# Performance work log

Hardware: AMD Instinct MI355X
Metric: run time of the kernel (lower is better)

The kernel has to match this reference:

```python
import jax, jax.numpy as jnp
from jax import lax
import numpy as np

W = 64          # net_width
NITER = 10
THRESH = 1e-3
MSTEP = 1.0


def setup_inputs() -> dict:
    key = jax.random.key(0)
    ks = jax.random.split(key, 10)
    B, Nh, DIM = 8, 16384, 1024
    eye = jnp.eye(W, dtype=jnp.float32)
    return {
        'y_re': jax.random.normal(ks[0], (B, 1, Nh), jnp.float32),
        'y_im': jax.random.normal(ks[1], (B, 1, Nh), jnp.float32),
        'H_re': jax.random.normal(ks[2], (32768, DIM), jnp.float32) / np.sqrt(DIM),
        'H_im': jax.random.normal(ks[3], (32768, DIM), jnp.float32) / np.sqrt(DIM),
        # torch inits: estep.weight=I, estep.bias=0, update.weight=I, memory.weight=1e-6*I;
        # add small perturbations so the math is non-degenerate.
        'estep_w': eye + 0.05 * jax.random.normal(ks[4], (W, W), jnp.float32),
        'estep_b': jnp.zeros((W,), jnp.float32),
        'update_w': eye + 0.05 * jax.random.normal(ks[5], (W, W), jnp.float32),
        'update_b': 0.02 * jax.random.normal(ks[6], (W,), jnp.float32),
        'memory_w': 1e-6 * eye + 0.01 * jax.random.normal(ks[7], (W, W), jnp.float32),
        'memory_b': 0.02 * jax.random.normal(ks[8], (W,), jnp.float32),
    }


def _forward(y_re, y_im, H_re, H_im, estep_w, estep_b, update_w, update_b, memory_w, memory_b):
    y = (y_re + 1j * y_im).astype(jnp.complex64)          # [B,1,Nh]
    y = jnp.concatenate([y, jnp.conj(y)], axis=2)         # [B,1,N]
    H = (H_re + 1j * H_im).astype(jnp.complex64)          # [N,DIM]
    B, N = y.shape[0], y.shape[2]
    DIM = H.shape[1]
    nb = N // W
    Hb = H.reshape(nb, W, DIM)                            # [nb,W,DIM]
    yb = y.reshape(B, nb, W).transpose(1, 0, 2)[:, :, None, :]  # [nb,B,1,W]

    x0 = jnp.zeros((B, 1, DIM), jnp.complex64)
    tau0 = jnp.ones((nb, B, 1, W), jnp.float32)

    def block_step(xk, blk):
        H_i, y_i, tau_i = blk                              # [W,DIM], [B,1,W], [B,1,W]
        zk = jnp.einsum('bod,wd->bow', xk, H_i)            # [B,1,W] complex
        r = y_i - zk
        a2 = jnp.abs(r) ** 2                               # [B,1,W] float32
        # expectation_step: xt / std(xt) (torch.std = unbiased, global)
        xt = a2 / jnp.std(a2, ddof=1)
        ht = jax.nn.sigmoid(xt @ estep_w.T + estep_b)
        tau_new = jax.nn.relu(ht @ update_w.T + update_b + tau_i @ memory_w.T + memory_b)
        sigma2 = jnp.mean(a2, axis=2, keepdims=True)       # [B,1,1]
        residual = MSTEP * r * tau_new / sigma2            # complex
        xk = xk + jnp.einsum('bow,wd->bod', residual, jnp.conj(H_i)) / (W * DIM)
        return xk, tau_new

    def iteration(carry, _):
        xk, tau = carry
        xk, tau_new = lax.scan(block_step, xk, (Hb, yb, tau))  # sequential over blocks
        # soft threshold: sgn(x) * relu(|x| - threshold * max|x|)
        ax = jnp.abs(xk)
        m = jnp.max(ax)
        sgn = jnp.where(ax > 0, xk / jnp.where(ax > 0, ax, 1.0), 0.0 + 0.0j)
        xk = sgn * jax.nn.relu(ax - THRESH * m)
        return (xk, tau_new), None

    (xk, tau), _ = lax.scan(iteration, (x0, tau0), None, length=NITER)
    tau_out = tau[:, :, 0, :].transpose(1, 0, 2)           # [B,nb,W]
    return jnp.real(xk), tau_out


def reference(y_re, y_im, H_re, H_im, estep_w, estep_b, update_w, update_b, memory_w, memory_b):
    return _forward(y_re, y_im, H_re, H_im, estep_w, estep_b,
                    update_w, update_b, memory_w, memory_b)
```

## Files before the change

kernel.cpp:

```cpp
#include <hip/hip_runtime.h>
#include <math.h>

#define NT  256
#define NWG 64
#define SCOPE_AG __HIP_MEMORY_SCOPE_AGENT

__device__ __forceinline__ float ld_f(const float* p) {
    return __hip_atomic_load(p, __ATOMIC_RELAXED, SCOPE_AG);
}
__device__ __forceinline__ void st_f(float* p, float v) {
    __hip_atomic_store(p, v, __ATOMIC_RELAXED, SCOPE_AG);
}
__device__ __forceinline__ unsigned ld_u(const unsigned* p) {
    return __hip_atomic_load(p, __ATOMIC_RELAXED, SCOPE_AG);
}
__device__ __forceinline__ void st_u(unsigned* p, unsigned v) {
    __hip_atomic_store(p, v, __ATOMIC_RELAXED, SCOPE_AG);
}
__device__ __forceinline__ float2 ld_f2(const float2* p) {
    unsigned long long u = __hip_atomic_load((const unsigned long long*)p, __ATOMIC_RELAXED, SCOPE_AG);
    float2 r;
    r.x = __uint_as_float((unsigned)u);
    r.y = __uint_as_float((unsigned)(u >> 32));
    return r;
}
__device__ __forceinline__ void st_f2(float2* p, float2 v) {
    unsigned long long u = ((unsigned long long)__float_as_uint(v.y) << 32) | (unsigned long long)__float_as_uint(v.x);
    __hip_atomic_store((unsigned long long*)p, u, __ATOMIC_RELAXED, SCOPE_AG);
}

__device__ __forceinline__ float wsum64(float v) {
    #pragma unroll
    for (int m = 1; m < 64; m <<= 1) v += __shfl_xor(v, m);
    return v;
}
__device__ __forceinline__ float wmax64(float v) {
    #pragma unroll
    for (int m = 1; m < 64; m <<= 1) v = fmaxf(v, __shfl_xor(v, m));
    return v;
}


__launch_bounds__(NT, 1)
__global__ void robii_kernel(
    const float* __restrict__ y_re, const float* __restrict__ y_im,
    const float* __restrict__ H_re, const float* __restrict__ H_im,
    const float* __restrict__ estep_w, const float* __restrict__ estep_b,
    const float* __restrict__ update_w, const float* __restrict__ update_b,
    const float* __restrict__ memory_w, const float* __restrict__ memory_b,
    float* __restrict__ out, float* __restrict__ ws)
{
    __shared__ float wTe[4096], wTu[4096], wTm[4096];
    __shared__ float be[64], bu[64], bm[64];
    __shared__ float a2s[512];
    __shared__ float redl[8];
    __shared__ float gmax[1];
    __shared__ float2 rown[64];
    __shared__ float xts[64], hts[64], taurow[64];
    __shared__ float2 resid[64];
    __shared__ float2 cpartC[4][32][4];
    __shared__ float2 x_l[128];

    float* mpartf = (float*)cpartC;

    const int g = blockIdx.x, t = threadIdx.x;
    const int c = g & 7;
    const int b = g >> 3;
    const int lane = t & 63, wv = t >> 6;
    const int sub = t & 31;
    const int rbase = t >> 5;

    float2*   partws = (float2*)ws;
    float*    tauws  = ws + 16384;
    float*    pmws   = ws + 278528;
    unsigned* flags  = (unsigned*)(ws + 278592);

    for (int i = t; i < 4096; i += NT) {
        int j = i >> 6, k = i & 63;
        wTe[k * 64 + j] = estep_w[i];
        wTu[k * 64 + j] = update_w[i];
        wTm[k * 64 + j] = memory_w[i];
    }
    if (t < 64) { be[t] = estep_b[t]; bu[t] = update_b[t]; bm[t] = memory_b[t]; taurow[t] = 1.0f; }
    if (t < 128) x_l[t] = make_float2(0.0f, 0.0f);
    for (int i = t; i < 4096; i += NT) st_f(&tauws[g * 4096 + i], 1.0f);

    unsigned ep = 1;
    {
        unsigned* plane = flags + ((ep & 1u) << 9);
        __syncthreads();
        if (t == 0) st_u(&plane[g * 8], ep);
        if (t < 64) {
            while (ld_u(&plane[t * 8]) != ep) __builtin_amdgcn_s_sleep(1);
        }
        __syncthreads();
    }

    const size_t hcol = (size_t)c * 128 + (size_t)sub * 4;

    float4 hAre[8], hAim[8], hBre[8], hBim[8];

#define PREF(DRE, DIM_, BLKN) do {                                                   \
        const float* _pr = H_re + ((size_t)(BLKN) * 64 + rbase) * 1024 + hcol;       \
        const float* _pi = H_im + ((size_t)(BLKN) * 64 + rbase) * 1024 + hcol;       \
        _Pragma("unroll")                                                            \
        for (int _j = 0; _j < 8; ++_j) {                                             \
            DRE[_j]  = *(const float4*)(_pr + (size_t)_j * 8192);                    \
            DIM_[_j] = *(const float4*)(_pi + (size_t)_j * 8192);                    \
        }                                                                            \
    } while (0)

    PREF(hAre, hAim, 0);

#define STEP(BLK, CRE, CIM, NRE, NIM) do {                                           \
        const int blk = (BLK);                                                       \
        const int par = blk & 1;                                                     \
        __syncthreads();                               \
            \
        float2 xr0 = x_l[sub * 4 + 0], xr1 = x_l[sub * 4 + 1];                       \
        float2 xr2 = x_l[sub * 4 + 2], xr3 = x_l[sub * 4 + 3];                       \
        _Pragma("unroll")                                                            \
        for (int j = 0; j < 8; ++j) {                                                \
            float4 hr = CRE[j], hi = CIM[j];                                         \
            float sr, si;                                                            \
            sr  = xr0.x * hr.x - xr0.y * hi.x;  si  = xr0.x * hi.x + xr0.y * hr.x;   \
            sr += xr1.x * hr.y - xr1.y * hi.y;  si += xr1.x * hi.y + xr1.y * hr.y;   \
            sr += xr2.x * hr.z - xr2.y * hi.z;  si += xr2.x * hi.z + xr2.y * hr.z;   \
            sr += xr3.x * hr.w - xr3.y * hi.w;  si += xr3.x * hi.w + xr3.y * hr.w;   \
            _Pragma("unroll")                                                        \
            for (int m = 1; m < 32; m <<= 1) {                                       \
                sr += __shfl_xor(sr, m); si += __shfl_xor(si, m);                    \
            }                                                                        \
            if (sub == 0)                                                            \
                st_f2(&partws[par * 4096 + (b * 64 + rbase + 8 * j) * 8 + c],        \
                      make_float2(sr, si));                                          \
        }                                                                            \
        ++ep;                                                                        \
        unsigned* plane = flags + ((ep & 1u) << 9);                                  \
                       \
        __syncthreads();                                                             \
        if (t == 0) st_u(&plane[g * 8], ep);                                         \
                \
        PREF(NRE, NIM, ((blk + 1) & 511));                                           \
        float tau_nxt = 0.0f;                                                        \
        if (t < 64) tau_nxt = ld_f(&tauws[(((blk + 1) & 511) * 8 + b) * 64 + t]);    \
        float yAr, yAi, yBr, yBi;                                                    \
        {                                                                            \
            int b1 = t >> 6, w1 = t & 63, n1 = blk * 64 + w1;                        \
            if (n1 < 16384) { yAr = y_re[b1 * 16384 + n1];         yAi = y_im[b1 * 16384 + n1]; } \
            else            { yAr = y_re[b1 * 16384 + n1 - 16384]; yAi = -y_im[b1 * 16384 + n1 - 16384]; } \
            int i2 = t + 256;                                                        \
            int b2 = i2 >> 6, w2 = i2 & 63, n2 = blk * 64 + w2;                      \
            if (n2 < 16384) { yBr = y_re[b2 * 16384 + n2];         yBi = y_im[b2 * 16384 + n2]; } \
            else            { yBr = y_re[b2 * 16384 + n2 - 16384]; yBi = -y_im[b2 * 16384 + n2 - 16384]; } \
        }                                                                            \
                \
        if (t < 64) {                                                                \
            while (ld_u(&plane[t * 8]) != ep) __builtin_amdgcn_s_sleep(1);           \
        }                                                                            \
        __syncthreads();                                                             \
                                      \
        _Pragma("unroll")                                                            \
        for (int e = 0; e < 2; ++e) {                                                \
            int idx = t + e * 256;                                                   \
            int b1 = idx >> 6, w = idx & 63;                                         \
            const float2* pp = partws + (size_t)par * 4096 + (size_t)idx * 8;        \
            float zr = 0.0f, zi = 0.0f;                                              \
            _Pragma("unroll")                                                        \
            for (int cc = 0; cc < 8; ++cc) {                                         \
                float2 v = ld_f2(pp + cc);                                           \
                zr += v.x; zi += v.y;                                                \
            }                                                                        \
            float rr = ((e == 0) ? yAr : yBr) - zr;                                  \
            float ri = ((e == 0) ? yAi : yBi) - zi;                                  \
            a2s[idx] = rr * rr + ri * ri;                                            \
            if (b1 == b) rown[w] = make_float2(rr, ri);                              \
        }                                                                            \
        __syncthreads();                                                             \
                                       \
        float va = a2s[t] + a2s[t + 256];                                            \
        float s_ = wsum64(va);                                                       \
        if (lane == 0) redl[wv] = s_;                                                \
        __syncthreads();                                                             \
        float mean = (redl[0] + redl[1] + redl[2] + redl[3]) * (1.0f / 512.0f);      \
        float d0 = a2s[t] - mean, d1 = a2s[t + 256] - mean;                          \
        float s2_ = wsum64(d0 * d0 + d1 * d1);                                       \
        float sg  = wsum64(a2s[b * 64 + lane]) * (1.0f / 64.0f);                     \
        if (lane == 0) redl[4 + wv] = s2_;                                           \
        __syncthreads();                                                             \
        float stdv = sqrtf((redl[4] + redl[5] + redl[6] + redl[7]) * (1.0f / 511.0f)); \
        if (t < 64) xts[t] = a2s[b * 64 + t] / stdv;                                 \
        __syncthreads();                                                             \
          \
        {                                                                            \
            int j = t & 63, q = t >> 6;                                              \
            float acc = 0.0f;                                                        \
            _Pragma("unroll")                                                        \
            for (int k16 = 0; k16 < 16; ++k16) {                                     \
                int k = q * 16 + k16;                                                \
                acc += wTe[k * 64 + j] * xts[k];                                     \
            }                                                                        \
            mpartf[q * 64 + j] = acc;                                                \
        }                                                                            \
        __syncthreads();                                                             \
        if (t < 64) {                                                                \
            float acc = be[t] + mpartf[t] + mpartf[64 + t] + mpartf[128 + t] + mpartf[192 + t]; \
            hts[t] = 1.0f / (1.0f + expf(-acc));                                     \
        }                                                                            \
        __syncthreads();                                                             \
                          \
        {                                                                            \
            int j = t & 63, q = t >> 6;                                              \
            float acc = 0.0f;                                                        \
            _Pragma("unroll")                                                        \
            for (int k16 = 0; k16 < 16; ++k16) {                                     \
                int k = q * 16 + k16;                                                \
                acc += wTu[k * 64 + j] * hts[k] + wTm[k * 64 + j] * taurow[k];       \
            }                                                                        \
            mpartf[q * 64 + j] = acc;                                                \
        }                                                                            \
        __syncthreads();                                                             \
        if (t < 64) {                                                                \
            float tn = bu[t] + bm[t] + mpartf[t] + mpartf[64 + t] + mpartf[128 + t] + mpartf[192 + t]; \
            tn = fmaxf(tn, 0.0f);                                                    \
            if (c == 0) st_f(&tauws[(blk * 8 + b) * 64 + t], tn);                    \
            float2 rv = rown[t];                                                     \
            float scl = tn / sg;                                                     \
            resid[t] = make_float2(rv.x * scl, rv.y * scl);                          \
        }                                                                            \
        __syncthreads();                                                             \
            \
        float2 ac0 = make_float2(0.f, 0.f), ac1 = make_float2(0.f, 0.f);             \
        float2 ac2 = make_float2(0.f, 0.f), ac3 = make_float2(0.f, 0.f);             \
        _Pragma("unroll")                                                            \
        for (int j = 0; j < 8; ++j) {                                                \
            float2 rs = resid[rbase + 8 * j];                                        \
            float4 hr = CRE[j], hi = CIM[j];                                         \
            ac0.x += rs.x * hr.x + rs.y * hi.x;  ac0.y += rs.y * hr.x - rs.x * hi.x; \
            ac1.x += rs.x * hr.y + rs.y * hi.y;  ac1.y += rs.y * hr.y - rs.x * hi.y; \
            ac2.x += rs.x * hr.z + rs.y * hi.z;  ac2.y += rs.y * hr.z - rs.x * hi.z; \
            ac3.x += rs.x * hr.w + rs.y * hi.w;  ac3.y += rs.y * hr.w - rs.x * hi.w; \
        }                                                                            \
        ac0.x += __shfl_xor(ac0.x, 32); ac0.y += __shfl_xor(ac0.y, 32);              \
        ac1.x += __shfl_xor(ac1.x, 32); ac1.y += __shfl_xor(ac1.y, 32);              \
        ac2.x += __shfl_xor(ac2.x, 32); ac2.y += __shfl_xor(ac2.y, 32);              \
        ac3.x += __shfl_xor(ac3.x, 32); ac3.y += __shfl_xor(ac3.y, 32);              \
        if ((t & 32) == 0) {                                                         \
            cpartC[wv][sub][0] = ac0; cpartC[wv][sub][1] = ac1;                      \
            cpartC[wv][sub][2] = ac2; cpartC[wv][sub][3] = ac3;                      \
        }                                                                            \
        if (t < 64) taurow[t] = tau_nxt;                  \
        __syncthreads();                                                             \
        if (t < 128) {                                                               \
            int sl = t >> 2, kk = t & 3;                                             \
            float2 s0 = cpartC[0][sl][kk], s1 = cpartC[1][sl][kk];                   \
            float2 s2 = cpartC[2][sl][kk], s3 = cpartC[3][sl][kk];                   \
            float2 xv = x_l[t];                                                      \
            xv.x += (s0.x + s1.x + s2.x + s3.x) * (1.0f / 65536.0f);                 \
            xv.y += (s0.y + s1.y + s2.y + s3.y) * (1.0f / 65536.0f);                 \
            x_l[t] = xv;                                                             \
        }                                                                            \
    } while (0)

    #pragma unroll 1
    for (int iter = 0; iter < 10; ++iter) {
        #pragma unroll 1
        for (int blk2 = 0; blk2 < 512; blk2 += 2) {
            STEP(blk2,     hAre, hAim, hBre, hBim);
            STEP(blk2 + 1, hBre, hBim, hAre, hAim);
        }

        float lm = 0.0f;
        if (t < 128) { float2 xv = x_l[t]; lm = sqrtf(xv.x * xv.x + xv.y * xv.y); }
        lm = wmax64(lm);
        if (lane == 0) redl[wv] = lm;
        __syncthreads();
        if (t == 0) st_f(&pmws[g], fmaxf(fmaxf(redl[0], redl[1]), fmaxf(redl[2], redl[3])));
        ++ep;
        {
            unsigned* plane = flags + ((ep & 1u) << 9);
            __syncthreads();
            if (t == 0) st_u(&plane[g * 8], ep);
            if (t < 64) {
                while (ld_u(&plane[t * 8]) != ep) __builtin_amdgcn_s_sleep(1);
            }
            __syncthreads();
        }
        float pv = (t < 64) ? ld_f(&pmws[t]) : 0.0f;
        pv = wmax64(pv);
        if (t == 0) gmax[0] = pv;
        __syncthreads();
        float m = gmax[0];
        if (t < 128) {
            float2 xv = x_l[t];
            float ax = sqrtf(xv.x * xv.x + xv.y * xv.y);
            float s = (ax > 0.0f) ? fmaxf(ax - 1e-3f * m, 0.0f) / ax : 0.0f;
            x_l[t] = make_float2(xv.x * s, xv.y * s);
        }
        __syncthreads();
    }

    if (t < 128) out[b * 1024 + c * 128 + t] = x_l[t].x;
    for (int i = g * 8; i < g * 8 + 8; ++i) {
        for (int idx = t; idx < 512; idx += NT) {
            int bb = idx >> 6, w = idx & 63;
            out[8192 + bb * 32768 + i * 64 + w] = ld_f(&tauws[(i * 8 + bb) * 64 + w]);
        }
    }
#undef STEP
#undef PREF
}

__global__ void robii_diag_kernel(float* out, int code) {
    int i = blockIdx.x * blockDim.x + threadIdx.x;
    if (i < 8192) out[i] = 1.0e6f * (float)(1 + code);
}

extern "C" void kernel_launch(void* const* d_in, const int* in_sizes, int n_in,
                              void* d_out, int out_size, void* d_ws, size_t ws_size,
                              hipStream_t stream) {
    (void)in_sizes; (void)n_in; (void)out_size; (void)ws_size;
    const float* y_re     = (const float*)d_in[0];
    const float* y_im     = (const float*)d_in[1];
    const float* H_re     = (const float*)d_in[2];
    const float* H_im     = (const float*)d_in[3];
    const float* estep_w  = (const float*)d_in[4];
    const float* estep_b  = (const float*)d_in[5];
    const float* update_w = (const float*)d_in[6];
    const float* update_b = (const float*)d_in[7];
    const float* memory_w = (const float*)d_in[8];
    const float* memory_b = (const float*)d_in[9];
    float* outp = (float*)d_out;
    float* wsp  = (float*)d_ws;

    hipLaunchKernelGGL(robii_kernel, dim3(NWG), dim3(NT), 0, stream,
                       y_re, y_im, H_re, H_im, estep_w, estep_b,
                       update_w, update_b, memory_w, memory_b, outp, wsp);
    hipError_t e = hipGetLastError();
    if (e != hipSuccess) {
        hipLaunchKernelGGL(robii_diag_kernel, dim3(32), dim3(256), 0, stream,
                           outp, (int)e);
    }
}
```

Baseline: 39.18 ms.

## Replace per-block flag barrier with tagged partial sums and store tau as bf16

Removes the grid-wide flag barrier in each block step. Each partial dot-product value is now packed with an epoch tag in a 64-bit word, so readers spin until every tag matches instead of waiting on a separate flag plane. Tau state is also stored in workspace as packed bf16 pairs, which halves its traffic. The cost is lower precision in tau, both in the recurrence and in the output, plus more polling loads per value and twice as many stores for partials.

```diff
diff --git a/kernel.cpp b/kernel.cpp
--- a/kernel.cpp
+++ b/kernel.cpp
@@ -4,6 +4,7 @@
 #define NT  256
 #define NWG 64
 #define SCOPE_AG __HIP_MEMORY_SCOPE_AGENT
+typedef unsigned long long ull;
 
 __device__ __forceinline__ float ld_f(const float* p) {
     return __hip_atomic_load(p, __ATOMIC_RELAXED, SCOPE_AG);
@@ -17,17 +18,24 @@
 __device__ __forceinline__ void st_u(unsigned* p, unsigned v) {
     __hip_atomic_store(p, v, __ATOMIC_RELAXED, SCOPE_AG);
 }
-__device__ __forceinline__ float2 ld_f2(const float2* p) {
-    unsigned long long u = __hip_atomic_load((const unsigned long long*)p, __ATOMIC_RELAXED, SCOPE_AG);
-    float2 r;
-    r.x = __uint_as_float((unsigned)u);
-    r.y = __uint_as_float((unsigned)(u >> 32));
-    return r;
-}
-__device__ __forceinline__ void st_f2(float2* p, float2 v) {
-    unsigned long long u = ((unsigned long long)__float_as_uint(v.y) << 32) | (unsigned long long)__float_as_uint(v.x);
-    __hip_atomic_store((unsigned long long*)p, u, __ATOMIC_RELAXED, SCOPE_AG);
-}
+__device__ __forceinline__ ull ld_u64(const ull* p) {
+    return __hip_atomic_load(p, __ATOMIC_RELAXED, SCOPE_AG);
+}
+__device__ __forceinline__ void st_u64(ull* p, ull v) {
+    __hip_atomic_store(p, v, __ATOMIC_RELAXED, SCOPE_AG);
+}
+__device__ __forceinline__ ull pack_tf(unsigned tag, float v) {
+    return ((ull)__float_as_uint(v) << 32) | (ull)tag;
+}
+__device__ __forceinline__ float hi_f(ull u) { return __uint_as_float((unsigned)(u >> 32)); }
+
+__device__ __forceinline__ unsigned bf16pack(float even, float odd) {
+    unsigned ua = __float_as_uint(even); ua += 0x7FFFu + ((ua >> 16) & 1u);
+    unsigned ub = __float_as_uint(odd);  ub += 0x7FFFu + ((ub >> 16) & 1u);
+    return (ua >> 16) | (ub & 0xFFFF0000u);
+}
+__device__ __forceinline__ float bf16lo(unsigned w) { return __uint_as_float(w << 16); }
+__device__ __forceinline__ float bf16hi(unsigned w) { return __uint_as_float(w & 0xFFFF0000u); }
 
 __device__ __forceinline__ float wsum64(float v) {
     #pragma unroll
@@ -70,10 +78,10 @@
     const int sub = t & 31;
     const int rbase = t >> 5;
 
-    float2*   partws = (float2*)ws;
-    float*    tauws  = ws + 16384;
-    float*    pmws   = ws + 278528;
-    unsigned* flags  = (unsigned*)(ws + 278592);
+    ull*      partuw = (ull*)ws;
+    unsigned* tau32  = (unsigned*)(ws + 32768);
+    float*    pmws   = ws + 163840;
+    unsigned* flags  = (unsigned*)(ws + 163904);
 
     for (int i = t; i < 4096; i += NT) {
         int j = i >> 6, k = i & 63;
@@ -83,7 +91,11 @@
     }
     if (t < 64) { be[t] = estep_b[t]; bu[t] = update_b[t]; bm[t] = memory_b[t]; taurow[t] = 1.0f; }
     if (t < 128) x_l[t] = make_float2(0.0f, 0.0f);
-    for (int i = t; i < 4096; i += NT) st_f(&tauws[g * 4096 + i], 1.0f);
+    for (int i = t; i < 2048; i += NT) st_u(&tau32[g * 2048 + i], 0x3F803F80u);
+    {
+        int par_i = t >> 7, w_i = (t >> 1) & 63, reim = t & 1;
+        st_u64(&partuw[((size_t)par_i * 512 + b * 64 + w_i) * 16 + (size_t)c * 2 + reim], 0ull);
+    }
 
     unsigned ep = 1;
     {
@@ -115,8 +127,9 @@
 #define STEP(BLK, CRE, CIM, NRE, NIM) do {                                           \
         const int blk = (BLK);                                                       \
         const int par = blk & 1;                                                     \
+        const unsigned stag = (unsigned)(iter * 512 + blk + 1);                      \
         __syncthreads();                               \
-            \
+              \
         float2 xr0 = x_l[sub * 4 + 0], xr1 = x_l[sub * 4 + 1];                       \
         float2 xr2 = x_l[sub * 4 + 2], xr3 = x_l[sub * 4 + 3];                       \
         _Pragma("unroll")                                                            \
@@ -131,19 +144,16 @@
             for (int m = 1; m < 32; m <<= 1) {                                       \
                 sr += __shfl_xor(sr, m); si += __shfl_xor(si, m);                    \
             }                                                                        \
-            if (sub == 0)                                                            \
-                st_f2(&partws[par * 4096 + (b * 64 + rbase + 8 * j) * 8 + c],        \
-                      make_float2(sr, si));                                          \
-        }                                                                            \
-        ++ep;                                                                        \
-        unsigned* plane = flags + ((ep & 1u) << 9);                                  \
-                       \
-        __syncthreads();                                                             \
-        if (t == 0) st_u(&plane[g * 8], ep);                                         \
-                \
+            ull* pw = partuw + ((size_t)par * 512 + b * 64 + rbase + 8 * j) * 16     \
+                             + (size_t)c * 2;                                        \
+            if (sub == 0)      st_u64(pw,     pack_tf(stag, sr));                    \
+            else if (sub == 1) st_u64(pw + 1, pack_tf(stag, si));                    \
+        }                                                                            \
+             \
         PREF(NRE, NIM, ((blk + 1) & 511));                                           \
-        float tau_nxt = 0.0f;                                                        \
-        if (t < 64) tau_nxt = ld_f(&tauws[(((blk + 1) & 511) * 8 + b) * 64 + t]);    \
+        unsigned tauw = 0;                                                           \
+        if (t < 64)                                                                  \
+            tauw = ld_u(&tau32[(((blk + 1) & 511) * 8 + b) * 32 + (t >> 1)]);        \
         float yAr, yAi, yBr, yBi;                                                    \
         {                                                                            \
             int b1 = t >> 6, w1 = t & 63, n1 = blk * 64 + w1;                        \
@@ -154,26 +164,35 @@
             if (n2 < 16384) { yBr = y_re[b2 * 16384 + n2];         yBi = y_im[b2 * 16384 + n2]; } \
             else            { yBr = y_re[b2 * 16384 + n2 - 16384]; yBi = -y_im[b2 * 16384 + n2 - 16384]; } \
         }                                                                            \
-                \
-        if (t < 64) {                                                                \
-            while (ld_u(&plane[t * 8]) != ep) __builtin_amdgcn_s_sleep(1);           \
-        }                                                                            \
-        __syncthreads();                                                             \
-                                      \
+             \
         _Pragma("unroll")                                                            \
         for (int e = 0; e < 2; ++e) {                                                \
             int idx = t + e * 256;                                                   \
-            int b1 = idx >> 6, w = idx & 63;                                         \
-            const float2* pp = partws + (size_t)par * 4096 + (size_t)idx * 8;        \
+            const ull* pb = partuw + ((size_t)par * 512 + idx) * 16;                 \
             float zr = 0.0f, zi = 0.0f;                                              \
             _Pragma("unroll")                                                        \
-            for (int cc = 0; cc < 8; ++cc) {                                         \
-                float2 v = ld_f2(pp + cc);                                           \
-                zr += v.x; zi += v.y;                                                \
+            for (int h = 0; h < 2; ++h) {                                            \
+                const ull* pc = pb + h * 8;                                          \
+                ull v0, v1, v2, v3, v4, v5, v6, v7;                                  \
+                bool ok = false;                                                     \
+                while (!ok) {                                                        \
+                    v0 = ld_u64(pc + 0); v1 = ld_u64(pc + 1);                        \
+                    v2 = ld_u64(pc + 2); v3 = ld_u64(pc + 3);                        \
+                    v4 = ld_u64(pc + 4); v5 = ld_u64(pc + 5);                        \
+                    v6 = ld_u64(pc + 6); v7 = ld_u64(pc + 7);                        \
+                    ok = ((unsigned)v0 == stag) & ((unsigned)v1 == stag)             \
+                       & ((unsigned)v2 == stag) & ((unsigned)v3 == stag)             \
+                       & ((unsigned)v4 == stag) & ((unsigned)v5 == stag)             \
+                       & ((unsigned)v6 == stag) & ((unsigned)v7 == stag);            \
+                    if (!ok) __builtin_amdgcn_s_sleep(1);                            \
+                }                                                                    \
+                zr += hi_f(v0) + hi_f(v2) + hi_f(v4) + hi_f(v6);                     \
+                zi += hi_f(v1) + hi_f(v3) + hi_f(v5) + hi_f(v7);                     \
             }                                                                        \
             float rr = ((e == 0) ? yAr : yBr) - zr;                                  \
             float ri = ((e == 0) ? yAi : yBi) - zi;                                  \
             a2s[idx] = rr * rr + ri * ri;                                            \
+            int b1 = idx >> 6, w = idx & 63;                                         \
             if (b1 == b) rown[w] = make_float2(rr, ri);                              \
         }                                                                            \
         __syncthreads();                                                             \
@@ -191,7 +210,7 @@
         float stdv = sqrtf((redl[4] + redl[5] + redl[6] + redl[7]) * (1.0f / 511.0f)); \
         if (t < 64) xts[t] = a2s[b * 64 + t] / stdv;                                 \
         __syncthreads();                                                             \
-          \
+                                \
         {                                                                            \
             int j = t & 63, q = t >> 6;                                              \
             float acc = 0.0f;                                                        \
@@ -223,7 +242,9 @@
         if (t < 64) {                                                                \
             float tn = bu[t] + bm[t] + mpartf[t] + mpartf[64 + t] + mpartf[128 + t] + mpartf[192 + t]; \
             tn = fmaxf(tn, 0.0f);                                                    \
-            if (c == 0) st_f(&tauws[(blk * 8 + b) * 64 + t], tn);                    \
+            float tno = __shfl_xor(tn, 1);                                           \
+            if (c == 0 && (t & 1) == 0)                                              \
+                st_u(&tau32[(blk * 8 + b) * 32 + (t >> 1)], bf16pack(tn, tno));      \
             float2 rv = rown[t];                                                     \
             float scl = tn / sg;                                                     \
             resid[t] = make_float2(rv.x * scl, rv.y * scl);                          \
@@ -249,7 +270,8 @@
             cpartC[wv][sub][0] = ac0; cpartC[wv][sub][1] = ac1;                      \
             cpartC[wv][sub][2] = ac2; cpartC[wv][sub][3] = ac3;                      \
         }                                                                            \
-        if (t < 64) taurow[t] = tau_nxt;                  \
+        if (t < 64)                         \
+            taurow[t] = (t & 1) ? bf16hi(tauw) : bf16lo(tauw);                       \
         __syncthreads();                                                             \
         if (t < 128) {                                                               \
             int sl = t >> 2, kk = t & 3;                                             \
@@ -304,7 +326,8 @@
     for (int i = g * 8; i < g * 8 + 8; ++i) {
         for (int idx = t; idx < 512; idx += NT) {
             int bb = idx >> 6, w = idx & 63;
-            out[8192 + bb * 32768 + i * 64 + w] = ld_f(&tauws[(i * 8 + bb) * 64 + w]);
+            unsigned uw = ld_u(&tau32[(i * 8 + bb) * 32 + (w >> 1)]);
+            out[8192 + bb * 32768 + i * 64 + w] = (w & 1) ? bf16hi(uw) : bf16lo(uw);
         }
     }
 #undef STEP
```

After: 61.26 ms. 56.3% more time.

## Replace flag barriers with tagged partial-sum data words for cross-workgroup sync

Applied to the files above, without the earlier changes.

Removes the per-block grid-wide flag barrier. Each partial z value now carries an 8-bit epoch tag in its low mantissa bits, and consumers spin until all eight tagged partials for their row match the expected tag. The per-iteration max exchange is tagged the same way. This drops a full barrier round trip per block step, at the cost of truncating 8 mantissa bits of the partial sums, which reduces precision, and of adding polling loads on the data itself.

```diff
diff --git a/kernel.cpp b/kernel.cpp
--- a/kernel.cpp
+++ b/kernel.cpp
@@ -4,6 +4,7 @@
 #define NT  256
 #define NWG 64
 #define SCOPE_AG __HIP_MEMORY_SCOPE_AGENT
+typedef unsigned long long ull;
 
 __device__ __forceinline__ float ld_f(const float* p) {
     return __hip_atomic_load(p, __ATOMIC_RELAXED, SCOPE_AG);
@@ -17,16 +18,21 @@
 __device__ __forceinline__ void st_u(unsigned* p, unsigned v) {
     __hip_atomic_store(p, v, __ATOMIC_RELAXED, SCOPE_AG);
 }
-__device__ __forceinline__ float2 ld_f2(const float2* p) {
-    unsigned long long u = __hip_atomic_load((const unsigned long long*)p, __ATOMIC_RELAXED, SCOPE_AG);
-    float2 r;
-    r.x = __uint_as_float((unsigned)u);
-    r.y = __uint_as_float((unsigned)(u >> 32));
-    return r;
-}
-__device__ __forceinline__ void st_f2(float2* p, float2 v) {
-    unsigned long long u = ((unsigned long long)__float_as_uint(v.y) << 32) | (unsigned long long)__float_as_uint(v.x);
-    __hip_atomic_store((unsigned long long*)p, u, __ATOMIC_RELAXED, SCOPE_AG);
+__device__ __forceinline__ void st_u_rel(unsigned* p, unsigned v) {
+    __hip_atomic_store(p, v, __ATOMIC_RELEASE, SCOPE_AG);
+}
+__device__ __forceinline__ ull ld_u64(const ull* p) {
+    return __hip_atomic_load(p, __ATOMIC_RELAXED, SCOPE_AG);
+}
+__device__ __forceinline__ void st_u64(ull* p, ull v) {
+    __hip_atomic_store(p, v, __ATOMIC_RELAXED, SCOPE_AG);
+}
+
+__device__ __forceinline__ unsigned tagf(float v, unsigned tg) {
+    return (__float_as_uint(v) & 0xFFFFFF00u) | tg;
+}
+__device__ __forceinline__ ull pack2(float lo, float hi, unsigned tg) {
+    return ((ull)tagf(hi, tg) << 32) | (ull)tagf(lo, tg);
 }
 
 __device__ __forceinline__ float wsum64(float v) {
@@ -70,10 +76,9 @@
     const int sub = t & 31;
     const int rbase = t >> 5;
 
-    float2*   partws = (float2*)ws;
+    ull*      partuw = (ull*)ws;
     float*    tauws  = ws + 16384;
-    float*    pmws   = ws + 278528;
-    unsigned* flags  = (unsigned*)(ws + 278592);
+    unsigned* pm_u   = (unsigned*)(ws + 278528);
 
     for (int i = t; i < 4096; i += NT) {
         int j = i >> 6, k = i & 63;
@@ -85,16 +90,13 @@
     if (t < 128) x_l[t] = make_float2(0.0f, 0.0f);
     for (int i = t; i < 4096; i += NT) st_f(&tauws[g * 4096 + i], 1.0f);
 
-    unsigned ep = 1;
-    {
-        unsigned* plane = flags + ((ep & 1u) << 9);
-        __syncthreads();
-        if (t == 0) st_u(&plane[g * 8], ep);
-        if (t < 64) {
-            while (ld_u(&plane[t * 8]) != ep) __builtin_amdgcn_s_sleep(1);
-        }
-        __syncthreads();
-    }
+    __syncthreads();
+    if (t == 0) st_u_rel(&pm_u[g], tagf(1.0f, 255u));
+    if (t < 64) {
+        while ((ld_u(&pm_u[t]) & 0xFFu) != 255u) __builtin_amdgcn_s_sleep(1);
+    }
+    __builtin_amdgcn_fence(__ATOMIC_ACQUIRE, "agent");
+    __syncthreads();
 
     const size_t hcol = (size_t)c * 128 + (size_t)sub * 4;
 
@@ -115,8 +117,10 @@
 #define STEP(BLK, CRE, CIM, NRE, NIM) do {                                           \
         const int blk = (BLK);                                                       \
         const int par = blk & 1;                                                     \
+        const unsigned tg = (unsigned)(iter * 512 + blk + 1) & 0xFFu;                \
         __syncthreads();                               \
-            \
+           \
+               \
         float2 xr0 = x_l[sub * 4 + 0], xr1 = x_l[sub * 4 + 1];                       \
         float2 xr2 = x_l[sub * 4 + 2], xr3 = x_l[sub * 4 + 3];                       \
         _Pragma("unroll")                                                            \
@@ -132,15 +136,10 @@
                 sr += __shfl_xor(sr, m); si += __shfl_xor(si, m);                    \
             }                                                                        \
             if (sub == 0)                                                            \
-                st_f2(&partws[par * 4096 + (b * 64 + rbase + 8 * j) * 8 + c],        \
-                      make_float2(sr, si));                                          \
-        }                                                                            \
-        ++ep;                                                                        \
-        unsigned* plane = flags + ((ep & 1u) << 9);                                  \
-                       \
-        __syncthreads();                                                             \
-        if (t == 0) st_u(&plane[g * 8], ep);                                         \
-                \
+                st_u64(&partuw[(size_t)par * 4096 + (b * 64 + rbase + 8 * j) * 8 + c], \
+                       pack2(sr, si, tg));                                           \
+        }                                                                            \
+                     \
         PREF(NRE, NIM, ((blk + 1) & 511));                                           \
         float tau_nxt = 0.0f;                                                        \
         if (t < 64) tau_nxt = ld_f(&tauws[(((blk + 1) & 511) * 8 + b) * 64 + t]);    \
@@ -154,26 +153,49 @@
             if (n2 < 16384) { yBr = y_re[b2 * 16384 + n2];         yBi = y_im[b2 * 16384 + n2]; } \
             else            { yBr = y_re[b2 * 16384 + n2 - 16384]; yBi = -y_im[b2 * 16384 + n2 - 16384]; } \
         }                                                                            \
-                \
-        if (t < 64) {                                                                \
-            while (ld_u(&plane[t * 8]) != ep) __builtin_amdgcn_s_sleep(1);           \
-        }                                                                            \
-        __syncthreads();                                                             \
-                                      \
+         \
         _Pragma("unroll")                                                            \
         for (int e = 0; e < 2; ++e) {                                                \
             int idx = t + e * 256;                                                   \
-            int b1 = idx >> 6, w = idx & 63;                                         \
-            const float2* pp = partws + (size_t)par * 4096 + (size_t)idx * 8;        \
-            float zr = 0.0f, zi = 0.0f;                                              \
-            _Pragma("unroll")                                                        \
-            for (int cc = 0; cc < 8; ++cc) {                                         \
-                float2 v = ld_f2(pp + cc);                                           \
-                zr += v.x; zi += v.y;                                                \
+            const ull* pb = partuw + (size_t)par * 4096 + (size_t)idx * 8;           \
+            ull v0, v1, v2, v3, v4, v5, v6, v7;                                      \
+            bool ok = false;                                                         \
+            while (!ok) {                                                            \
+                v0 = ld_u64(pb + 0); v1 = ld_u64(pb + 1);                            \
+                v2 = ld_u64(pb + 2); v3 = ld_u64(pb + 3);                            \
+                v4 = ld_u64(pb + 4); v5 = ld_u64(pb + 5);                            \
+                v6 = ld_u64(pb + 6); v7 = ld_u64(pb + 7);                            \
+                unsigned m01 = ((unsigned)v0 & 0xFFu) ^ tg;                          \
+                m01 |= ((unsigned)(v0 >> 32) & 0xFFu) ^ tg;                          \
+                m01 |= ((unsigned)v1 & 0xFFu) ^ tg;                                  \
+                m01 |= ((unsigned)(v1 >> 32) & 0xFFu) ^ tg;                          \
+                m01 |= ((unsigned)v2 & 0xFFu) ^ tg;                                  \
+                m01 |= ((unsigned)(v2 >> 32) & 0xFFu) ^ tg;                          \
+                m01 |= ((unsigned)v3 & 0xFFu) ^ tg;                                  \
+                m01 |= ((unsigned)(v3 >> 32) & 0xFFu) ^ tg;                          \
+                m01 |= ((unsigned)v4 & 0xFFu) ^ tg;                                  \
+                m01 |= ((unsigned)(v4 >> 32) & 0xFFu) ^ tg;                          \
+                m01 |= ((unsigned)v5 & 0xFFu) ^ tg;                                  \
+                m01 |= ((unsigned)(v5 >> 32) & 0xFFu) ^ tg;                          \
+                m01 |= ((unsigned)v6 & 0xFFu) ^ tg;                                  \
+                m01 |= ((unsigned)(v6 >> 32) & 0xFFu) ^ tg;                          \
+                m01 |= ((unsigned)v7 & 0xFFu) ^ tg;                                  \
+                m01 |= ((unsigned)(v7 >> 32) & 0xFFu) ^ tg;                          \
+                ok = (m01 == 0u);                                                    \
+                if (!ok) __builtin_amdgcn_s_sleep(1);                                \
             }                                                                        \
+            float zr = __uint_as_float((unsigned)v0) + __uint_as_float((unsigned)v1) \
+                     + __uint_as_float((unsigned)v2) + __uint_as_float((unsigned)v3) \
+                     + __uint_as_float((unsigned)v4) + __uint_as_float((unsigned)v5) \
+                     + __uint_as_float((unsigned)v6) + __uint_as_float((unsigned)v7);\
+            float zi = __uint_as_float((unsigned)(v0 >> 32)) + __uint_as_float((unsigned)(v1 >> 32)) \
+                     + __uint_as_float((unsigned)(v2 >> 32)) + __uint_as_float((unsigned)(v3 >> 32)) \
+                     + __uint_as_float((unsigned)(v4 >> 32)) + __uint_as_float((unsigned)(v5 >> 32)) \
+                     + __uint_as_float((unsigned)(v6 >> 32)) + __uint_as_float((unsigned)(v7 >> 32));\
             float rr = ((e == 0) ? yAr : yBr) - zr;                                  \
             float ri = ((e == 0) ? yAi : yBi) - zi;                                  \
             a2s[idx] = rr * rr + ri * ri;                                            \
+            int b1 = idx >> 6, w = idx & 63;                                         \
             if (b1 == b) rown[w] = make_float2(rr, ri);                              \
         }                                                                            \
         __syncthreads();                                                             \
@@ -191,7 +213,7 @@
         float stdv = sqrtf((redl[4] + redl[5] + redl[6] + redl[7]) * (1.0f / 511.0f)); \
         if (t < 64) xts[t] = a2s[b * 64 + t] / stdv;                                 \
         __syncthreads();                                                             \
-          \
+                                \
         {                                                                            \
             int j = t & 63, q = t >> 6;                                              \
             float acc = 0.0f;                                                        \
@@ -270,23 +292,25 @@
             STEP(blk2 + 1, hBre, hBim, hAre, hAim);
         }
 
+        const unsigned itg = (unsigned)(iter + 1);
         float lm = 0.0f;
         if (t < 128) { float2 xv = x_l[t]; lm = sqrtf(xv.x * xv.x + xv.y * xv.y); }
         lm = wmax64(lm);
         if (lane == 0) redl[wv] = lm;
         __syncthreads();
-        if (t == 0) st_f(&pmws[g], fmaxf(fmaxf(redl[0], redl[1]), fmaxf(redl[2], redl[3])));
-        ++ep;
-        {
-            unsigned* plane = flags + ((ep & 1u) << 9);
-            __syncthreads();
-            if (t == 0) st_u(&plane[g * 8], ep);
-            if (t < 64) {
-                while (ld_u(&plane[t * 8]) != ep) __builtin_amdgcn_s_sleep(1);
+        if (t == 0)
+            st_u_rel(&pm_u[g], tagf(fmaxf(fmaxf(redl[0], redl[1]), fmaxf(redl[2], redl[3])), itg));
+        float pv = 0.0f;
+        if (t < 64) {
+            unsigned u;
+            for (;;) {
+                u = ld_u(&pm_u[t]);
+                if ((u & 0xFFu) == itg) break;
+                __builtin_amdgcn_s_sleep(1);
             }
-            __syncthreads();
+            pv = __uint_as_float(u);
         }
-        float pv = (t < 64) ? ld_f(&pmws[t]) : 0.0f;
+        __builtin_amdgcn_fence(__ATOMIC_ACQUIRE, "agent");
         pv = wmax64(pv);
         if (t == 0) gmax[0] = pv;
         __syncthreads();
```

New measurement: 37.74 ms. -3.7%, faster.
